# Kernel tuning notes

Hardware: AMD Instinct MI355X
Metric: run time of the kernel (lower is better)

## Reference

```python
import jax, jax.numpy as jnp
import numpy as np

N = 50000
H = 4
C = 32  # hidden_channels // heads
NEG_SLOPE = 0.2


def gat_layer(x, W, a_src, a_dst, b, src, dst):
    # x: [N, F_in]; W: [F_in, H*C]; a_src/a_dst: [H, C]; b: [H*C]
    h = (x @ W).reshape(N, H, C)                      # [N, H, C]
    alpha_src = jnp.sum(h * a_src, axis=-1)           # [N, H]
    alpha_dst = jnp.sum(h * a_dst, axis=-1)           # [N, H]
    e = jax.nn.leaky_relu(alpha_src[src] + alpha_dst[dst], NEG_SLOPE)  # [E, H]
    # softmax over incoming edges per destination node (stable)
    m = jax.ops.segment_max(e, dst, num_segments=N)   # [N, H]
    p = jnp.exp(e - m[dst])                           # [E, H]
    s = jax.ops.segment_sum(p, dst, num_segments=N)   # [N, H]
    alpha = p / s[dst]                                # [E, H]
    msg = h[src] * alpha[:, :, None]                  # [E, H, C]
    out = jax.ops.segment_sum(msg, dst, num_segments=N)  # [N, H, C]
    return out.reshape(N, H * C) + b


def setup_inputs() -> dict:
    key = jax.random.key(0)
    ks = jax.random.split(key, 12)
    E = 1600000
    x = jax.random.normal(ks[0], (N, 128), dtype=jnp.float32)
    edge_index = jax.random.randint(ks[1], (2, E), 0, N, dtype=jnp.int32)
    s = 0.08
    return {
        "x": x,
        "edge_index": edge_index,
        "W1": jax.random.normal(ks[2], (128, H * C), dtype=jnp.float32) * s,
        "a_src1": jax.random.normal(ks[3], (H, C), dtype=jnp.float32) * s,
        "a_dst1": jax.random.normal(ks[4], (H, C), dtype=jnp.float32) * s,
        "b1": jnp.zeros((H * C,), dtype=jnp.float32),
        "W2": jax.random.normal(ks[5], (H * C, H * C), dtype=jnp.float32) * s,
        "a_src2": jax.random.normal(ks[6], (H, C), dtype=jnp.float32) * s,
        "a_dst2": jax.random.normal(ks[7], (H, C), dtype=jnp.float32) * s,
        "b2": jnp.zeros((H * C,), dtype=jnp.float32),
    }


def reference(x, edge_index, W1, a_src1, a_dst1, b1, W2, a_src2, a_dst2, b2):
    # PyG GATConv default add_self_loops=True: append (i -> i) edges
    loops = jnp.arange(N, dtype=edge_index.dtype)
    src = jnp.concatenate([edge_index[0], loops])
    dst = jnp.concatenate([edge_index[1], loops])
    # layer 1 + ELU (dropout is identity in eval mode)
    h = gat_layer(x, W1, a_src1, a_dst1, b1, src, dst)
    h = jax.nn.elu(h)
    # layer 2 + ELU
    h = gat_layer(h, W2, a_src2, a_dst2, b2, src, dst)
    h = jax.nn.elu(h)
    return h
```

## Files before the change

kernel.cpp:

```cpp
#include <hip/hip_runtime.h>
#include <hip/hip_bf16.h>

static __device__ __forceinline__ float bf2f_lo(unsigned u) {
    return __uint_as_float(u << 16);
}
static __device__ __forceinline__ float bf2f_hi(unsigned u) {
    return __uint_as_float(u & 0xffff0000u);
}
static __device__ __forceinline__ unsigned f2bf_rne_bits(float f) {
    unsigned u = __float_as_uint(f);
    return u + 0x7fffu + ((u >> 16) & 1u);
}
static __device__ __forceinline__ unsigned pack_bf2(float a, float b) {
    return (f2bf_rne_bits(a) >> 16) | (f2bf_rne_bits(b) & 0xffff0000u);
}


#define CHUNK 4096

__global__ void kb_zero(int* bucketCount, int NBK) {
    int i = blockIdx.x * 256 + threadIdx.x;
    if (i < NBK) bucketCount[i] = 0;
}

__global__ void kb_count(const int* __restrict__ dst, int* bucketCount,
                         int E, int T, int NBK) {
    __shared__ int cnt[256];
    const int tid = threadIdx.x;
    const int beg = blockIdx.x * CHUNK;
    const int end = min(beg + CHUNK, T);
    cnt[tid] = 0;
    __syncthreads();
    for (int i = beg + tid; i < end; i += 256) {
        int d = (i < E) ? dst[i] : (i - E);
        atomicAdd(&cnt[d >> 8], 1);
    }
    __syncthreads();
    if (tid < NBK && cnt[tid] > 0) atomicAdd(&bucketCount[tid], cnt[tid]);
}

__global__ void kb_scan(const int* __restrict__ bucketCount, int* bucketBase,
                        int* bucketCursor, int* row_ptr, int NBK, int N, int total) {
    __shared__ int sm[256];
    const int tid = threadIdx.x;
    int v = (tid < NBK) ? bucketCount[tid] : 0;
    sm[tid] = v;
    __syncthreads();
    for (int off = 1; off < 256; off <<= 1) {
        int t = (tid >= off) ? sm[tid - off] : 0;
        __syncthreads();
        sm[tid] += t;
        __syncthreads();
    }
    if (tid < NBK) {
        int ex = sm[tid] - v;
        bucketBase[tid] = ex;
        bucketCursor[tid] = ex;
    }
    if (tid == 0) {
        bucketBase[NBK] = total;
        row_ptr[N] = total;
    }
}

__global__ void kb_place(const int* __restrict__ src, const int* __restrict__ dst,
                         int* bucketCursor, unsigned* __restrict__ barr,
                         int E, int T, int NBK) {
    __shared__ int cnt[256];
    __shared__ int wb[256];
    const int tid = threadIdx.x;
    const int beg = blockIdx.x * CHUNK;
    const int end = min(beg + CHUNK, T);
    cnt[tid] = 0;
    __syncthreads();
    for (int i = beg + tid; i < end; i += 256) {
        int d = (i < E) ? dst[i] : (i - E);
        atomicAdd(&cnt[d >> 8], 1);
    }
    __syncthreads();
    if (tid < NBK) {
        int c = cnt[tid];
        wb[tid] = (c > 0) ? atomicAdd(&bucketCursor[tid], c) : 0;
    }
    __syncthreads();
    cnt[tid] = 0;
    __syncthreads();
    for (int i = beg + tid; i < end; i += 256) {
        int s, d;
        if (i < E) { s = src[i]; d = dst[i]; }
        else       { s = i - E;  d = s; }
        int g = d >> 8;
        unsigned pk = (unsigned)s | ((unsigned)(d & 255) << 16);
        int r = atomicAdd(&cnt[g], 1);
        barr[wb[g] + r] = pk;
    }
}

__global__ void kb_csr(const unsigned* __restrict__ barr, const int* __restrict__ bucketBase,
                       int* __restrict__ row_ptr, int* __restrict__ col, int N) {
    __shared__ int cnt[256];
    __shared__ int sm[256];
    __shared__ int cur[256];
    const int tid = threadIdx.x;
    const int b = blockIdx.x;
    const int beg = bucketBase[b];
    const int end = bucketBase[b + 1];
    cnt[tid] = 0;
    __syncthreads();
    for (int i = beg + tid; i < end; i += 256)
        atomicAdd(&cnt[barr[i] >> 16], 1);
    __syncthreads();
    int v = cnt[tid];
    sm[tid] = v;
    __syncthreads();
    for (int off = 1; off < 256; off <<= 1) {
        int t = (tid >= off) ? sm[tid - off] : 0;
        __syncthreads();
        sm[tid] += t;
        __syncthreads();
    }
    int ex = sm[tid] - v;
    int n = b * 256 + tid;
    if (n < N) row_ptr[n] = beg + ex;
    cur[tid] = beg + ex;
    __syncthreads();
    for (int i = beg + tid; i < end; i += 256) {
        unsigned p = barr[i];
        int pos = atomicAdd(&cur[p >> 16], 1);
        col[pos] = (int)(p & 0xFFFFu);
    }
}

#define KC 32
__launch_bounds__(512, 1)
__global__ void k_gemm(const float* __restrict__ A, const float* __restrict__ W,
                       const float* __restrict__ a_src, const float* __restrict__ a_dst,
                       unsigned* __restrict__ Hout,
                       float* __restrict__ asrc_o, float* __restrict__ adst_o,
                       int nrows) {
    __shared__ float Wl[KC * 128];
    __shared__ float Xl[128 * (KC + 4)];
    const int tid = threadIdx.x;
    const int tx = tid & 15;
    const int ty = tid >> 4;
    const int row0 = blockIdx.x * 128;

    float acc[4][8];
#pragma unroll
    for (int i = 0; i < 4; i++)
#pragma unroll
        for (int j = 0; j < 8; j++) acc[i][j] = 0.f;

    for (int kc = 0; kc < 128; kc += KC) {
#pragma unroll
        for (int it = 0; it < 2; ++it) {
            int ff = it * 512 + tid;
            int r = ff >> 5, cq = ff & 31;
            *(float4*)&Wl[r * 128 + cq * 4] = *(const float4*)&W[(size_t)(kc + r) * 128 + cq * 4];
        }
#pragma unroll
        for (int it = 0; it < 2; ++it) {
            int ff = it * 512 + tid;
            int r = ff >> 3, kq = ff & 7;
            int gr = row0 + r;
            float4 v = make_float4(0.f, 0.f, 0.f, 0.f);
            if (gr < nrows) v = *(const float4*)&A[(size_t)gr * 128 + kc + kq * 4];
            *(float4*)&Xl[r * (KC + 4) + kq * 4] = v;
        }
        __syncthreads();
#pragma unroll
        for (int k0 = 0; k0 < KC; k0 += 4) {
            float4 xv[4];
#pragma unroll
            for (int i = 0; i < 4; i++)
                xv[i] = *(float4*)&Xl[(4 * ty + i) * (KC + 4) + k0];
            const float* xp = (const float*)xv;
#pragma unroll
            for (int kk = 0; kk < 4; ++kk) {
                float4 w0 = *(float4*)&Wl[(k0 + kk) * 128 + 8 * tx];
                float4 w1 = *(float4*)&Wl[(k0 + kk) * 128 + 8 * tx + 4];
#pragma unroll
                for (int i = 0; i < 4; i++) {
                    float xs = xp[i * 4 + kk];
                    acc[i][0] += xs * w0.x; acc[i][1] += xs * w0.y;
                    acc[i][2] += xs * w0.z; acc[i][3] += xs * w0.w;
                    acc[i][4] += xs * w1.x; acc[i][5] += xs * w1.y;
                    acc[i][6] += xs * w1.z; acc[i][7] += xs * w1.w;
                }
            }
        }
        __syncthreads();
    }

    const int head = tx >> 2;
    const int c0 = 8 * tx;
    float as_c[8], ad_c[8];
#pragma unroll
    for (int j = 0; j < 8; j++) { as_c[j] = a_src[c0 + j]; ad_c[j] = a_dst[c0 + j]; }
#pragma unroll
    for (int i = 0; i < 4; i++) {
        int gr = row0 + 4 * ty + i;
        float ps = 0.f, pd = 0.f;
#pragma unroll
        for (int j = 0; j < 8; j++) { ps += acc[i][j] * as_c[j]; pd += acc[i][j] * ad_c[j]; }
        ps += __shfl_xor(ps, 1); ps += __shfl_xor(ps, 2);
        pd += __shfl_xor(pd, 1); pd += __shfl_xor(pd, 2);
        if (gr < nrows) {
            if ((tx & 3) == 0) {
                asrc_o[(size_t)gr * 4 + head] = ps;
                adst_o[(size_t)gr * 4 + head] = pd;
            }
            uint4 o;
            o.x = pack_bf2(acc[i][0], acc[i][1]);
            o.y = pack_bf2(acc[i][2], acc[i][3]);
            o.z = pack_bf2(acc[i][4], acc[i][5]);
            o.w = pack_bf2(acc[i][6], acc[i][7]);
            *(uint4*)&Hout[(size_t)gr * 64 + 4 * tx] = o;
        }
    }
}

#define UAG 8
__launch_bounds__(256)
__global__ void k_aggr(const unsigned* __restrict__ h,
                       const float* __restrict__ asrc, const float* __restrict__ adst,
                       const float* __restrict__ bias,
                       const int* __restrict__ row_ptr, const int* __restrict__ col,
                       float* __restrict__ out, int N) {
    const int lane = threadIdx.x & 63;
    const int d = blockIdx.x * 4 + (threadIdx.x >> 6);
    if (d >= N) return;
    const int hd = lane >> 4;
    const float adv = adst[(size_t)d * 4 + hd];
    const int beg = row_ptr[d];
    const int end = row_ptr[d + 1];

    float ac0[2] = {0.f, 0.f}, ac1[2] = {0.f, 0.f}, sps[2] = {0.f, 0.f};
    int j = beg;
    for (; j + UAG <= end; j += UAG) {
        int s[UAG];
#pragma unroll
        for (int k = 0; k < UAG; ++k) s[k] = col[j + k];
        float av[UAG];
        unsigned uv[UAG];
#pragma unroll
        for (int k = 0; k < UAG; ++k) {
            av[k] = asrc[(size_t)s[k] * 4 + hd];
            uv[k] = h[(size_t)s[k] * 64 + lane];
        }
#pragma unroll
        for (int k = 0; k < UAG; ++k) {
            float e = av[k] + adv;
            e = (e > 0.f) ? e : 0.2f * e;
            float p = __expf(e);
            ac0[k & 1] += p * bf2f_lo(uv[k]);
            ac1[k & 1] += p * bf2f_hi(uv[k]);
            sps[k & 1] += p;
        }
    }
    for (; j < end; ++j) {
        int s = col[j];
        float e = asrc[(size_t)s * 4 + hd] + adv;
        e = (e > 0.f) ? e : 0.2f * e;
        float p = __expf(e);
        unsigned u = h[(size_t)s * 64 + lane];
        ac0[0] += p * bf2f_lo(u);
        ac1[0] += p * bf2f_hi(u);
        sps[0] += p;
    }
    float acc0 = ac0[0] + ac0[1];
    float acc1 = ac1[0] + ac1[1];
    float sp = sps[0] + sps[1];

    float inv = 1.f / sp;
    int c = 2 * lane;
    float v0 = acc0 * inv + bias[c];
    float v1 = acc1 * inv + bias[c + 1];
    v0 = (v0 > 0.f) ? v0 : (__expf(v0) - 1.f);
    v1 = (v1 > 0.f) ? v1 : (__expf(v1) - 1.f);
    *(float2*)&out[(size_t)d * 128 + c] = make_float2(v0, v1);
}

extern "C" void kernel_launch(void* const* d_in, const int* in_sizes, int n_in,
                              void* d_out, int out_size, void* d_ws, size_t ws_size,
                              hipStream_t stream) {
    const float* x      = (const float*)d_in[0];
    const int*   ei     = (const int*)d_in[1];
    const float* W1     = (const float*)d_in[2];
    const float* a_src1 = (const float*)d_in[3];
    const float* a_dst1 = (const float*)d_in[4];
    const float* b1     = (const float*)d_in[5];
    const float* W2     = (const float*)d_in[6];
    const float* a_src2 = (const float*)d_in[7];
    const float* a_dst2 = (const float*)d_in[8];
    const float* b2     = (const float*)d_in[9];

    const int N = in_sizes[0] / 128;
    const int E = in_sizes[1] / 2;
    const int T = E + N;
    const int NBK = (N + 255) / 256;
    const int* src = ei;
    const int* dst = ei + E;

    char* w = (char*)d_ws;
    auto alloc = [&](size_t bytes) -> char* {
        char* p = w;
        w += (bytes + 255) & ~(size_t)255;
        return p;
    };
    unsigned* h_bf    = (unsigned*)alloc((size_t)N * 64 * 4);
    float*    o1      = (float*)alloc((size_t)N * 128 * 4);
    float*    asrc    = (float*)alloc((size_t)N * 4 * 4);
    float*    adst    = (float*)alloc((size_t)N * 4 * 4);
    int*      row_ptr = (int*)alloc((size_t)(N + 1) * 4);
    int*      col     = (int*)alloc((size_t)T * 4);
    int*      bCount  = (int*)alloc((size_t)NBK * 4);
    int*      bBase   = (int*)alloc((size_t)(NBK + 1) * 4);
    int*      bCursor = (int*)alloc((size_t)NBK * 4);
    unsigned* barr    = (unsigned*)o1;
    (void)ws_size; (void)n_in; (void)out_size;

    const int PB = (T + CHUNK - 1) / CHUNK;

    hipLaunchKernelGGL(kb_zero, dim3((NBK + 255) / 256), dim3(256), 0, stream, bCount, NBK);
    hipLaunchKernelGGL(kb_count, dim3(PB), dim3(256), 0, stream, dst, bCount, E, T, NBK);
    hipLaunchKernelGGL(kb_scan, dim3(1), dim3(256), 0, stream, bCount, bBase, bCursor, row_ptr, NBK, N, T);
    hipLaunchKernelGGL(kb_place, dim3(PB), dim3(256), 0, stream, src, dst, bCursor, barr, E, T, NBK);
    hipLaunchKernelGGL(kb_csr, dim3(NBK), dim3(256), 0, stream, barr, bBase, row_ptr, col, N);

    const int GB = (N + 127) / 128;
    const int AB = (N + 3) / 4;

    hipLaunchKernelGGL(k_gemm, dim3(GB), dim3(512), 0, stream, x, W1, a_src1, a_dst1, h_bf, asrc, adst, N);
    hipLaunchKernelGGL(k_aggr, dim3(AB), dim3(256), 0, stream, h_bf, asrc, adst, b1, row_ptr, col, o1, N);
    hipLaunchKernelGGL(k_gemm, dim3(GB), dim3(512), 0, stream, o1, W2, a_src2, a_dst2, h_bf, asrc, adst, N);
    hipLaunchKernelGGL(k_aggr, dim3(AB), dim3(256), 0, stream, h_bf, asrc, adst, b2, row_ptr, col, (float*)d_out, N);
}
```

Before: 345.8 us.

## Precompute normalized edge attention in separate kernel before aggregation

```diff
diff --git a/kernel.cpp b/kernel.cpp
--- a/kernel.cpp
+++ b/kernel.cpp
@@ -1,5 +1,6 @@
 #include <hip/hip_runtime.h>
 #include <hip/hip_bf16.h>
+#include <hip/hip_fp16.h>
 
 static __device__ __forceinline__ float bf2f_lo(unsigned u) {
     return __uint_as_float(u << 16);
@@ -14,7 +15,10 @@
 static __device__ __forceinline__ unsigned pack_bf2(float a, float b) {
     return (f2bf_rne_bits(a) >> 16) | (f2bf_rne_bits(b) & 0xffff0000u);
 }
-
+static __device__ __forceinline__ float pfun(float e) {
+    e = fmaxf(e, 0.2f * e);
+    return __expf(e);
+}
 
 #define CHUNK 4096
 
@@ -220,62 +224,110 @@
     }
 }
 
+__launch_bounds__(256)
+__global__ void k_edge(const float* __restrict__ asrc, const float* __restrict__ adst,
+                       const int* __restrict__ row_ptr, const int* __restrict__ col,
+                       __half* __restrict__ alpha_t, int N, int T) {
+    const int wv = (blockIdx.x * 256 + threadIdx.x) >> 6;
+    const int lane = threadIdx.x & 63;
+    if (wv >= N) return;
+    const int beg = row_ptr[wv];
+    const int cnt = row_ptr[wv + 1] - beg;
+    const float4 ad = *(const float4*)&adst[(size_t)wv * 4];
+
+    float4 sp = make_float4(0.f, 0.f, 0.f, 0.f);
+    float4 p0 = make_float4(0.f, 0.f, 0.f, 0.f);
+    for (int base = 0; base < cnt; base += 64) {
+        float4 p = make_float4(0.f, 0.f, 0.f, 0.f);
+        if (base + lane < cnt) {
+            int s = col[beg + base + lane];
+            float4 av = *(const float4*)&asrc[(size_t)s * 4];
+            p.x = pfun(av.x + ad.x);
+            p.y = pfun(av.y + ad.y);
+            p.z = pfun(av.z + ad.z);
+            p.w = pfun(av.w + ad.w);
+        }
+        if (base == 0) p0 = p;
+        sp.x += p.x; sp.y += p.y; sp.z += p.z; sp.w += p.w;
+    }
+#pragma unroll
+    for (int off = 1; off < 64; off <<= 1) {
+        sp.x += __shfl_xor(sp.x, off);
+        sp.y += __shfl_xor(sp.y, off);
+        sp.z += __shfl_xor(sp.z, off);
+        sp.w += __shfl_xor(sp.w, off);
+    }
+    float4 inv = make_float4(1.f / sp.x, 1.f / sp.y, 1.f / sp.z, 1.f / sp.w);
+
+    for (int base = 0; base < cnt; base += 64) {
+        if (base + lane < cnt) {
+            int j = beg + base + lane;
+            float4 p;
+            if (base == 0) {
+                p = p0;
+            } else {
+                int s = col[j];
+                float4 av = *(const float4*)&asrc[(size_t)s * 4];
+                p.x = pfun(av.x + ad.x);
+                p.y = pfun(av.y + ad.y);
+                p.z = pfun(av.z + ad.z);
+                p.w = pfun(av.w + ad.w);
+            }
+            alpha_t[(size_t)0 * T + j] = __float2half(p.x * inv.x);
+            alpha_t[(size_t)1 * T + j] = __float2half(p.y * inv.y);
+            alpha_t[(size_t)2 * T + j] = __float2half(p.z * inv.z);
+            alpha_t[(size_t)3 * T + j] = __float2half(p.w * inv.w);
+        }
+    }
+}
+
 #define UAG 8
 __launch_bounds__(256)
 __global__ void k_aggr(const unsigned* __restrict__ h,
-                       const float* __restrict__ asrc, const float* __restrict__ adst,
+                       const __half* __restrict__ alpha_t,
                        const float* __restrict__ bias,
                        const int* __restrict__ row_ptr, const int* __restrict__ col,
-                       float* __restrict__ out, int N) {
+                       float* __restrict__ out, int N, int T) {
     const int lane = threadIdx.x & 63;
     const int d = blockIdx.x * 4 + (threadIdx.x >> 6);
     if (d >= N) return;
     const int hd = lane >> 4;
-    const float adv = adst[(size_t)d * 4 + hd];
+    const __half* at = alpha_t + (size_t)hd * T;
     const int beg = row_ptr[d];
     const int end = row_ptr[d + 1];
 
-    float ac0[2] = {0.f, 0.f}, ac1[2] = {0.f, 0.f}, sps[2] = {0.f, 0.f};
+    float ac0[2] = {0.f, 0.f}, ac1[2] = {0.f, 0.f};
     int j = beg;
     for (; j + UAG <= end; j += UAG) {
         int s[UAG];
 #pragma unroll
         for (int k = 0; k < UAG; ++k) s[k] = col[j + k];
-        float av[UAG];
+        float af[UAG];
         unsigned uv[UAG];
 #pragma unroll
         for (int k = 0; k < UAG; ++k) {
-            av[k] = asrc[(size_t)s[k] * 4 + hd];
+            af[k] = __half2float(at[j + k]);
             uv[k] = h[(size_t)s[k] * 64 + lane];
         }
 #pragma unroll
         for (int k = 0; k < UAG; ++k) {
-            float e = av[k] + adv;
-            e = (e > 0.f) ? e : 0.2f * e;
-            float p = __expf(e);
-            ac0[k & 1] += p * bf2f_lo(uv[k]);
-            ac1[k & 1] += p * bf2f_hi(uv[k]);
-            sps[k & 1] += p;
+            ac0[k & 1] += af[k] * bf2f_lo(uv[k]);
+            ac1[k & 1] += af[k] * bf2f_hi(uv[k]);
         }
     }
     for (; j < end; ++j) {
         int s = col[j];
-        float e = asrc[(size_t)s * 4 + hd] + adv;
-        e = (e > 0.f) ? e : 0.2f * e;
-        float p = __expf(e);
+        float a = __half2float(at[j]);
         unsigned u = h[(size_t)s * 64 + lane];
-        ac0[0] += p * bf2f_lo(u);
-        ac1[0] += p * bf2f_hi(u);
-        sps[0] += p;
+        ac0[0] += a * bf2f_lo(u);
+        ac1[0] += a * bf2f_hi(u);
     }
     float acc0 = ac0[0] + ac0[1];
     float acc1 = ac1[0] + ac1[1];
-    float sp = sps[0] + sps[1];
-
-    float inv = 1.f / sp;
+
     int c = 2 * lane;
-    float v0 = acc0 * inv + bias[c];
-    float v1 = acc1 * inv + bias[c + 1];
+    float v0 = acc0 + bias[c];
+    float v1 = acc1 + bias[c + 1];
     v0 = (v0 > 0.f) ? v0 : (__expf(v0) - 1.f);
     v1 = (v1 > 0.f) ? v1 : (__expf(v1) - 1.f);
     *(float2*)&out[(size_t)d * 128 + c] = make_float2(v0, v1);
@@ -314,6 +366,7 @@
     float*    adst    = (float*)alloc((size_t)N * 4 * 4);
     int*      row_ptr = (int*)alloc((size_t)(N + 1) * 4);
     int*      col     = (int*)alloc((size_t)T * 4);
+    __half*   alpha_t = (__half*)alloc((size_t)T * 4 * 2);
     int*      bCount  = (int*)alloc((size_t)NBK * 4);
     int*      bBase   = (int*)alloc((size_t)(NBK + 1) * 4);
     int*      bCursor = (int*)alloc((size_t)NBK * 4);
@@ -330,9 +383,12 @@
 
     const int GB = (N + 127) / 128;
     const int AB = (N + 3) / 4;
+    const int EB = (N * 64 + 255) / 256;
 
     hipLaunchKernelGGL(k_gemm, dim3(GB), dim3(512), 0, stream, x, W1, a_src1, a_dst1, h_bf, asrc, adst, N);
-    hipLaunchKernelGGL(k_aggr, dim3(AB), dim3(256), 0, stream, h_bf, asrc, adst, b1, row_ptr, col, o1, N);
+    hipLaunchKernelGGL(k_edge, dim3(EB), dim3(256), 0, stream, asrc, adst, row_ptr, col, alpha_t, N, T);
+    hipLaunchKernelGGL(k_aggr, dim3(AB), dim3(256), 0, stream, h_bf, alpha_t, b1, row_ptr, col, o1, N, T);
     hipLaunchKernelGGL(k_gemm, dim3(GB), dim3(512), 0, stream, o1, W2, a_src2, a_dst2, h_bf, asrc, adst, N);
-    hipLaunchKernelGGL(k_aggr, dim3(AB), dim3(256), 0, stream, h_bf, asrc, adst, b2, row_ptr, col, (float*)d_out, N);
-}
+    hipLaunchKernelGGL(k_edge, dim3(EB), dim3(256), 0, stream, asrc, adst, row_ptr, col, alpha_t, N, T);
+    hipLaunchKernelGGL(k_aggr, dim3(AB), dim3(256), 0, stream, h_bf, alpha_t, b2, row_ptr, col, (float*)d_out, N, T);
+}
```

Measured after the change: 372.6 us. 7.8% more time.

## Distribute per-edge attention exp across lanes and broadcast via shuffles in aggregation

Applied to the files above, without the earlier changes.

```diff
diff --git a/kernel.cpp b/kernel.cpp
--- a/kernel.cpp
+++ b/kernel.cpp
@@ -14,7 +14,10 @@
 static __device__ __forceinline__ unsigned pack_bf2(float a, float b) {
     return (f2bf_rne_bits(a) >> 16) | (f2bf_rne_bits(b) & 0xffff0000u);
 }
-
+static __device__ __forceinline__ float pfun(float e) {
+    e = fmaxf(e, 0.2f * e);
+    return __expf(e);
+}
 
 #define CHUNK 4096
 
@@ -220,7 +223,7 @@
     }
 }
 
-#define UAG 8
+#define BAT 16
 __launch_bounds__(256)
 __global__ void k_aggr(const unsigned* __restrict__ h,
                        const float* __restrict__ asrc, const float* __restrict__ adst,
@@ -230,52 +233,51 @@
     const int lane = threadIdx.x & 63;
     const int d = blockIdx.x * 4 + (threadIdx.x >> 6);
     if (d >= N) return;
-    const int hd = lane >> 4;
-    const float adv = adst[(size_t)d * 4 + hd];
+    const int eb  = lane >> 2;
+    const int hp  = lane & 3;
+    const int hdc = lane >> 4;
+    const float adv = adst[(size_t)d * 4 + hp];
     const int beg = row_ptr[d];
     const int end = row_ptr[d + 1];
 
-    float ac0[2] = {0.f, 0.f}, ac1[2] = {0.f, 0.f}, sps[2] = {0.f, 0.f};
-    int j = beg;
-    for (; j + UAG <= end; j += UAG) {
-        int s[UAG];
-#pragma unroll
-        for (int k = 0; k < UAG; ++k) s[k] = col[j + k];
-        float av[UAG];
-        unsigned uv[UAG];
-#pragma unroll
-        for (int k = 0; k < UAG; ++k) {
-            av[k] = asrc[(size_t)s[k] * 4 + hd];
-            uv[k] = h[(size_t)s[k] * 64 + lane];
-        }
-#pragma unroll
-        for (int k = 0; k < UAG; ++k) {
-            float e = av[k] + adv;
-            e = (e > 0.f) ? e : 0.2f * e;
-            float p = __expf(e);
-            ac0[k & 1] += p * bf2f_lo(uv[k]);
-            ac1[k & 1] += p * bf2f_hi(uv[k]);
-            sps[k & 1] += p;
-        }
-    }
-    for (; j < end; ++j) {
-        int s = col[j];
-        float e = asrc[(size_t)s * 4 + hd] + adv;
-        e = (e > 0.f) ? e : 0.2f * e;
-        float p = __expf(e);
-        unsigned u = h[(size_t)s * 64 + lane];
-        ac0[0] += p * bf2f_lo(u);
-        ac1[0] += p * bf2f_hi(u);
-        sps[0] += p;
-    }
-    float acc0 = ac0[0] + ac0[1];
-    float acc1 = ac1[0] + ac1[1];
-    float sp = sps[0] + sps[1];
-
-    float inv = 1.f / sp;
+    float ac0 = 0.f, ac1 = 0.f, sp = 0.f;
+
+    int cv = 0;
+    { int idx = beg + eb; if (idx < end) cv = col[idx]; }
+
+    for (int j = beg; j < end; j += BAT) {
+        int cvn = 0;
+        { int idx = j + BAT + eb; if (idx < end) cvn = col[idx]; }
+
+        float a = asrc[(size_t)(unsigned)cv * 4 + hp];
+        float p = (j + eb < end) ? pfun(a + adv) : 0.f;
+        sp += p;
+
+        unsigned u[BAT];
+#pragma unroll
+        for (int k = 0; k < BAT; ++k) {
+            int sk = __builtin_amdgcn_readlane(cv, 4 * k);
+            u[k] = h[(size_t)(unsigned)sk * 64 + lane];
+        }
+#pragma unroll
+        for (int k = 0; k < BAT; ++k) {
+            float pk = __shfl(p, 4 * k + hdc);
+            ac0 += pk * bf2f_lo(u[k]);
+            ac1 += pk * bf2f_hi(u[k]);
+        }
+        cv = cvn;
+    }
+
+    sp += __shfl_xor(sp, 4);
+    sp += __shfl_xor(sp, 8);
+    sp += __shfl_xor(sp, 16);
+    sp += __shfl_xor(sp, 32);
+    float spv = __shfl(sp, hdc);
+    float inv = 1.f / spv;
+
     int c = 2 * lane;
-    float v0 = acc0 * inv + bias[c];
-    float v1 = acc1 * inv + bias[c + 1];
+    float v0 = ac0 * inv + bias[c];
+    float v1 = ac1 * inv + bias[c + 1];
     v0 = (v0 > 0.f) ? v0 : (__expf(v0) - 1.f);
     v1 = (v1 > 0.f) ? v1 : (__expf(v1) - 1.f);
     *(float2*)&out[(size_t)d * 128 + c] = make_float2(v0, v1);
```

Result: faster. 329.2 us (-4.8%).
